# Performance work log

Measured on AMD Instinct MI355X. Metric: run time of the kernel, lower is better.

Reference implementation:

```python
import jax, jax.numpy as jnp
import numpy as np

FEATS = 1024
HEAD = 16
MLP_HIDDEN = 4096
HEAD_DIM = FEATS // HEAD
SQRT_D = float(FEATS) ** 0.5  # module scales by sqrt(feats), not sqrt(head_dim)
LN_EPS = 1e-5


def layer_norm(x, g, b):
    mu = jnp.mean(x, axis=-1, keepdims=True)
    var = jnp.mean(jnp.square(x - mu), axis=-1, keepdims=True)
    return (x - mu) * jax.lax.rsqrt(var + LN_EPS) * g + b


def setup_inputs() -> dict:
    key = jax.random.key(0)
    ks = jax.random.split(key, 12)
    s = 1.0 / np.sqrt(FEATS)
    s2 = 1.0 / np.sqrt(MLP_HIDDEN)
    return {
        "x": jax.random.normal(ks[0], (2, 2048, FEATS), dtype=jnp.float32),
        "ln1_g": jnp.ones((FEATS,), jnp.float32),
        "ln1_b": jnp.zeros((FEATS,), jnp.float32),
        "wq": jax.random.normal(ks[1], (FEATS, FEATS), jnp.float32) * s,
        "bq": jnp.zeros((FEATS,), jnp.float32),
        "wk": jax.random.normal(ks[2], (FEATS, FEATS), jnp.float32) * s,
        "bk": jnp.zeros((FEATS,), jnp.float32),
        "wv": jax.random.normal(ks[3], (FEATS, FEATS), jnp.float32) * s,
        "bv": jnp.zeros((FEATS,), jnp.float32),
        "wo": jax.random.normal(ks[4], (FEATS, FEATS), jnp.float32) * s,
        "bo": jnp.zeros((FEATS,), jnp.float32),
        "ln2_g": jnp.ones((FEATS,), jnp.float32),
        "ln2_b": jnp.zeros((FEATS,), jnp.float32),
        "w1": jax.random.normal(ks[5], (MLP_HIDDEN, FEATS), jnp.float32) * s,
        "b1": jnp.zeros((MLP_HIDDEN,), jnp.float32),
        "w2": jax.random.normal(ks[6], (FEATS, MLP_HIDDEN), jnp.float32) * s2,
        "b2": jnp.zeros((FEATS,), jnp.float32),
    }


def reference(x, ln1_g, ln1_b, wq, bq, wk, bk, wv, bv, wo, bo,
              ln2_g, ln2_b, w1, b1, w2, b2):
    b, n, f = x.shape
    h = layer_norm(x, ln1_g, ln1_b)
    # qkv projections (torch Linear: y = x @ W.T + b)
    q = (h @ wq.T + bq).reshape(b, n, HEAD, HEAD_DIM).transpose(0, 2, 1, 3)
    k = (h @ wk.T + bk).reshape(b, n, HEAD, HEAD_DIM).transpose(0, 2, 1, 3)
    v = (h @ wv.T + bv).reshape(b, n, HEAD, HEAD_DIM).transpose(0, 2, 1, 3)
    score = jax.nn.softmax(jnp.einsum('bhif,bhjf->bhij', q, k) / SQRT_D, axis=-1)
    attn = jnp.einsum('bhij,bhjf->bihf', score, v).reshape(b, n, f)
    o = attn @ wo.T + bo
    out1 = o + x
    h2 = layer_norm(out1, ln2_g, ln2_b)
    mlp = jax.nn.relu(jax.nn.relu(h2 @ w1.T + b1) @ w2.T + b2)
    return mlp + out1
```

## Files before the change

### kernel.cpp

```cpp
#include <hip/hip_runtime.h>
#include <hip/hip_bf16.h>

#define FEATS 1024
#define NH 16
#define HD 64
#define SEQ 2048
#define BATCH 2
#define MTOT (BATCH*SEQ)
#define MLPH 4096
#define QSCALE 0.04508422277369218f

typedef __attribute__((ext_vector_type(8))) short bf16x8;
typedef __attribute__((ext_vector_type(4))) short bf16x4;
typedef __attribute__((ext_vector_type(4))) float f32x4;

static_assert(sizeof(bf16x8) == 16, "bf16x8 must be 16B");

__device__ __forceinline__ unsigned short f2bf(float f) {
    unsigned int u = __float_as_uint(f);
    unsigned int lsb = (u >> 16) & 1u;
    u += 0x7fffu + lsb;
    return (unsigned short)(u >> 16);
}

#define ASYNC16(GP, LP) __builtin_amdgcn_global_load_lds( \
    (const __attribute__((address_space(1))) void*)(GP),  \
    (__attribute__((address_space(3))) void*)(LP), 16, 0, 0)

__global__ __launch_bounds__(256) void cvt_kernel(const float* __restrict__ src,
                                                  unsigned short* __restrict__ dst,
                                                  int n, float scale) {
    int i = (blockIdx.x * 256 + threadIdx.x) * 4;
    if (i + 3 < n) {
        float4 v = *(const float4*)(src + i);
        ushort4 o;
        o.x = f2bf(v.x * scale); o.y = f2bf(v.y * scale);
        o.z = f2bf(v.z * scale); o.w = f2bf(v.w * scale);
        *(ushort4*)(dst + i) = o;
    }
}

__global__ __launch_bounds__(256) void concat3_kernel(const float* __restrict__ a,
                                                      const float* __restrict__ b,
                                                      const float* __restrict__ c,
                                                      float* __restrict__ o) {
    int i = blockIdx.x * 256 + threadIdx.x;
    float v = (i < 1024) ? a[i] * QSCALE : ((i < 2048) ? b[i - 1024] : c[i - 2048]);
    o[i] = v;
}

__global__ __launch_bounds__(256) void ln_kernel(const float* __restrict__ x,
                                                 const float* __restrict__ g,
                                                 const float* __restrict__ bta,
                                                 unsigned short* __restrict__ h) {
    __shared__ float red[8];
    const int row = blockIdx.x;
    const int t = threadIdx.x;
    const float* xr = x + (size_t)row * FEATS;
    float4 v = ((const float4*)xr)[t];
    float s  = v.x + v.y + v.z + v.w;
    float ss = v.x * v.x + v.y * v.y + v.z * v.z + v.w * v.w;
#pragma unroll
    for (int off = 1; off < 64; off <<= 1) {
        s  += __shfl_xor(s, off);
        ss += __shfl_xor(ss, off);
    }
    const int w = t >> 6;
    if ((t & 63) == 0) { red[w] = s; red[4 + w] = ss; }
    __syncthreads();
    s  = red[0] + red[1] + red[2] + red[3];
    ss = red[4] + red[5] + red[6] + red[7];
    const float mu  = s * (1.f / FEATS);
    const float var = ss * (1.f / FEATS) - mu * mu;
    const float rs  = rsqrtf(var + 1e-5f);
    float4 gv = ((const float4*)g)[t];
    float4 bv = ((const float4*)bta)[t];
    ushort4 ov;
    ov.x = f2bf((v.x - mu) * rs * gv.x + bv.x);
    ov.y = f2bf((v.y - mu) * rs * gv.y + bv.y);
    ov.z = f2bf((v.z - mu) * rs * gv.z + bv.z);
    ov.w = f2bf((v.w - mu) * rs * gv.w + bv.w);
    ((ushort4*)h)[(size_t)row * (FEATS / 4) + t] = ov;
}

template <bool RELU, bool ADD, bool OUTBF16>
__global__ __launch_bounds__(256, 3)
void gemm_kernel(const unsigned short* __restrict__ A,
                 const unsigned short* __restrict__ W,
                 const float* __restrict__ bias,
                 const float* __restrict__ addend,
                 void* __restrict__ outp,
                 int M, int N, int K, int gx) {
    __shared__ unsigned short lds[3][2][128 * 32];

    const int t = threadIdx.x;
    const int w = t >> 6, lane = t & 63;
    const int wr = w >> 1, wc = w & 1;
    const int li = lane & 15, lj = lane >> 4;

    const int nwg = gridDim.x;
    const int cpx = nwg >> 3;
    const int wg = blockIdx.x;
    const int swz = (wg & 7) * cpx + (wg >> 3);
    const int mb = (swz / gx) * 128, nb = (swz % gx) * 128;

    const int srow = lane >> 2, sc = (lane & 3) * 8;
    const unsigned short* gA = A + (size_t)(mb + w * 16 + srow) * K + sc;
    const unsigned short* gB = W + (size_t)(nb + w * 16 + srow) * K + sc;
    const size_t half = (size_t)64 * K;
    const int lbase = w * 512 + lane * 8;

    const int nt = K >> 5;

#define STAGE(BUF, K0)                                             \
    do {                                                           \
        unsigned short* la_ = &lds[BUF][0][lbase];                 \
        unsigned short* lb_ = &lds[BUF][1][lbase];                 \
        ASYNC16(gA + (K0), la_);                                   \
        ASYNC16(gA + half + (K0), la_ + 2048);                     \
        ASYNC16(gB + (K0), lb_);                                   \
        ASYNC16(gB + half + (K0), lb_ + 2048);                     \
    } while (0)

    STAGE(0, 0);
    STAGE(1, 32);
    asm volatile("s_waitcnt vmcnt(4)" ::: "memory");
    __builtin_amdgcn_s_barrier();

    f32x4 acc[4][4] = {};

    for (int i = 0; i < nt; ++i) {
        const int cur = i % 3;
        const unsigned short* Al = &lds[cur][0][0];
        const unsigned short* Bl = &lds[cur][1][0];

        bf16x8 af[4], bfr[4];
#pragma unroll
        for (int m = 0; m < 4; m++)
            af[m] = *(const bf16x8*)(Al + (wr * 64 + m * 16 + li) * 32 + lj * 8);
#pragma unroll
        for (int n = 0; n < 4; n++)
            bfr[n] = *(const bf16x8*)(Bl + (wc * 64 + n * 16 + li) * 32 + lj * 8);

        const int pf = i + 2 < nt;
        if (pf) STAGE((i + 2) % 3, (i + 2) * 32);

#pragma unroll
        for (int m = 0; m < 4; m++)
#pragma unroll
            for (int n = 0; n < 4; n++)
                acc[m][n] = __builtin_amdgcn_mfma_f32_16x16x32_bf16(af[m], bfr[n], acc[m][n], 0, 0, 0);

        if (i + 1 < nt) {
            if (pf) asm volatile("s_waitcnt vmcnt(4)" ::: "memory");
            else    asm volatile("s_waitcnt vmcnt(0)" ::: "memory");
            __builtin_amdgcn_s_barrier();
        }
    }
#undef STAGE

#pragma unroll
    for (int m = 0; m < 4; m++) {
#pragma unroll
        for (int n = 0; n < 4; n++) {
            const int col = nb + wc * 64 + n * 16 + li;
            const float bv = bias[col];
#pragma unroll
            for (int r = 0; r < 4; r++) {
                const int row = mb + wr * 64 + m * 16 + lj * 4 + r;
                float v = acc[m][n][r] + bv;
                if (RELU) v = fmaxf(v, 0.f);
                if (ADD)  v += addend[(size_t)row * N + col];
                if (OUTBF16)
                    ((unsigned short*)outp)[(size_t)row * N + col] = f2bf(v);
                else
                    ((float*)outp)[(size_t)row * N + col] = v;
            }
        }
    }
}

__global__ __launch_bounds__(256) void vtrans_kernel(const unsigned short* __restrict__ qkv,
                                                     unsigned short* __restrict__ vt) {
    constexpr int LDV = 68;
    __shared__ unsigned short Vl[64 * LDV];
    const int bh = blockIdx.x, st = blockIdx.y;
    const int b = bh >> 4, h = bh & 15;
    const int t = threadIdx.x;
    const unsigned short* src = qkv + (size_t)(b * SEQ + st * 64) * (3 * FEATS) + 2 * FEATS + h * HD;
#pragma unroll
    for (int i = 0; i < 2; i++) {
        int idx = t + i * 256;
        int r = idx >> 3, c = (idx & 7) * 8;
        *(bf16x8*)(Vl + r * LDV + c) = *(const bf16x8*)(src + (size_t)r * (3 * FEATS) + c);
    }
    __syncthreads();
    unsigned short* dst = vt + (size_t)bh * HD * SEQ + st * 64;
#pragma unroll
    for (int i = 0; i < 2; i++) {
        int idx = t + i * 256;
        int d = idx >> 3, s8 = (idx & 7) * 8;
        bf16x8 v;
#pragma unroll
        for (int j = 0; j < 8; j++) v[j] = Vl[(s8 + j) * LDV + d];
        *(bf16x8*)(dst + (size_t)d * SEQ + s8) = v;
    }
}

__global__ __launch_bounds__(512, 4)
void attn_kernel(const unsigned short* __restrict__ qkv,
                 const unsigned short* __restrict__ vt,
                 unsigned short* __restrict__ out) {
    constexpr int LK = 72;
    constexpr int LV = 136;
    __shared__ unsigned short Kl[2][128 * LK];
    __shared__ unsigned short Vtl[2][64 * LV];

    const int bh = blockIdx.y;
    const int b = bh >> 4, h = bh & 15;
    const int q0 = blockIdx.x * 128;
    const int t = threadIdx.x, w = t >> 6, lane = t & 63;
    const int li = lane & 15, lj = lane >> 4;

    const size_t rstr = 3 * FEATS;
    const unsigned short* qkvb = qkv + (size_t)(b * SEQ) * rstr;
    const unsigned short* ksrc = qkvb + FEATS + h * HD;
    const unsigned short* vsrc = vt + (size_t)bh * HD * SEQ;

    bf16x8 aq[2];
#pragma unroll
    for (int kk = 0; kk < 2; kk++)
        aq[kk] = *(const bf16x8*)(qkvb + (size_t)(q0 + w * 16 + li) * rstr + h * HD + kk * 32 + lj * 8);

    f32x4 o[4] = {};
    float lsum = 0.f;

    const int skey = t >> 2, sc = (t & 3) * 16;
    const unsigned short* kg = ksrc + (size_t)skey * rstr + sc;
    const int ldoK = skey * LK + sc;
    const int sd = t >> 3, c0 = (t & 7) * 16;
    const unsigned short* vg = vsrc + (size_t)sd * SEQ + c0;
    const int posA = (c0 & 96) | (((c0 >> 2) & 3) << 3) | (((c0 >> 4) & 1) << 2);
    const int ldoV = sd * LV + posA;

    const int nt = SEQ / 128;

#define VSPLIT(VR0, VR1, BUF)                                            \
    do {                                                                 \
        *(bf16x4*)(&Vtl[BUF][ldoV])      = __builtin_shufflevector(VR0, VR0, 0, 1, 2, 3); \
        *(bf16x4*)(&Vtl[BUF][ldoV + 8])  = __builtin_shufflevector(VR0, VR0, 4, 5, 6, 7); \
        *(bf16x4*)(&Vtl[BUF][ldoV + 16]) = __builtin_shufflevector(VR1, VR1, 0, 1, 2, 3); \
        *(bf16x4*)(&Vtl[BUF][ldoV + 24]) = __builtin_shufflevector(VR1, VR1, 4, 5, 6, 7); \
    } while (0)

    {
        bf16x8 k0 = *(const bf16x8*)kg;
        bf16x8 k1 = *(const bf16x8*)(kg + 8);
        bf16x8 v0 = *(const bf16x8*)vg;
        bf16x8 v1 = *(const bf16x8*)(vg + 8);
        *(bf16x8*)(&Kl[0][ldoK])     = k0;
        *(bf16x8*)(&Kl[0][ldoK + 8]) = k1;
        VSPLIT(v0, v1, 0);
    }

    int cur = 0;
    for (int i = 0; i < nt; ++i) {
        bf16x8 kr0, kr1, vr0, vr1;
        if (i + 1 < nt) {
            const unsigned short* kn = kg + (size_t)(i + 1) * 128 * rstr;
            const unsigned short* vn = vg + (i + 1) * 128;
            kr0 = *(const bf16x8*)kn;
            kr1 = *(const bf16x8*)(kn + 8);
            vr0 = *(const bf16x8*)vn;
            vr1 = *(const bf16x8*)(vn + 8);
        }

        asm volatile("s_waitcnt lgkmcnt(0)" ::: "memory");
        __builtin_amdgcn_s_barrier();

        const unsigned short* Kc = Kl[cur];
        const unsigned short* Vc = Vtl[cur];

        f32x4 s[8];
        __builtin_amdgcn_s_setprio(1);
#pragma unroll
        for (int n = 0; n < 8; n++) {
            bf16x8 k0 = *(const bf16x8*)(Kc + (n * 16 + li) * LK + lj * 8);
            bf16x8 k1 = *(const bf16x8*)(Kc + (n * 16 + li) * LK + 32 + lj * 8);
            f32x4 acc = {};
            acc = __builtin_amdgcn_mfma_f32_16x16x32_bf16(k0, aq[0], acc, 0, 0, 0);
            acc = __builtin_amdgcn_mfma_f32_16x16x32_bf16(k1, aq[1], acc, 0, 0, 0);
            s[n] = acc;
        }
        __builtin_amdgcn_s_setprio(0);

        bf16x8 A[4];
#pragma unroll
        for (int kk = 0; kk < 4; kk++) {
            float p[8];
#pragma unroll
            for (int r = 0; r < 4; r++) {
                p[r]     = exp2f(s[2 * kk][r]);
                p[4 + r] = exp2f(s[2 * kk + 1][r]);
                lsum += p[r] + p[4 + r];
            }
            union { unsigned u[4]; bf16x8 v; } Au;
            asm("v_cvt_pk_bf16_f32 %0, %1, %2" : "=v"(Au.u[0]) : "v"(p[0]), "v"(p[1]));
            asm("v_cvt_pk_bf16_f32 %0, %1, %2" : "=v"(Au.u[1]) : "v"(p[2]), "v"(p[3]));
            asm("v_cvt_pk_bf16_f32 %0, %1, %2" : "=v"(Au.u[2]) : "v"(p[4]), "v"(p[5]));
            asm("v_cvt_pk_bf16_f32 %0, %1, %2" : "=v"(Au.u[3]) : "v"(p[6]), "v"(p[7]));
            A[kk] = Au.v;
        }

        __builtin_amdgcn_s_setprio(1);
#pragma unroll
        for (int n = 0; n < 4; n++) {
#pragma unroll
            for (int kk = 0; kk < 4; kk++) {
                bf16x8 bv = *(const bf16x8*)(Vc + (n * 16 + li) * LV + kk * 32 + lj * 8);
                o[n] = __builtin_amdgcn_mfma_f32_16x16x32_bf16(A[kk], bv, o[n], 0, 0, 0);
            }
        }
        __builtin_amdgcn_s_setprio(0);

        if (i + 1 < nt) {
            *(bf16x8*)(&Kl[cur ^ 1][ldoK])     = kr0;
            *(bf16x8*)(&Kl[cur ^ 1][ldoK + 8]) = kr1;
            VSPLIT(vr0, vr1, cur ^ 1);
        }
        cur ^= 1;
    }
#undef VSPLIT

    lsum += __shfl_xor(lsum, 16);
    lsum += __shfl_xor(lsum, 32);
    const float dinv = 1.f / lsum;
    float inv[4];
#pragma unroll
    for (int r = 0; r < 4; r++)
        inv[r] = __shfl(dinv, lj * 4 + r);

    unsigned short* ob = out + (size_t)(b * SEQ + q0 + w * 16) * FEATS + h * HD;
#pragma unroll
    for (int n = 0; n < 4; n++)
#pragma unroll
        for (int r = 0; r < 4; r++)
            ob[(size_t)(lj * 4 + r) * FEATS + n * 16 + li] = f2bf(o[n][r] * inv[r]);
}

extern "C" void kernel_launch(void* const* d_in, const int* in_sizes, int n_in,
                              void* d_out, int out_size, void* d_ws, size_t ws_size,
                              hipStream_t stream) {
    const float* x     = (const float*)d_in[0];
    const float* ln1_g = (const float*)d_in[1];
    const float* ln1_b = (const float*)d_in[2];
    const float* wq    = (const float*)d_in[3];
    const float* bq    = (const float*)d_in[4];
    const float* wk    = (const float*)d_in[5];
    const float* bk    = (const float*)d_in[6];
    const float* wv    = (const float*)d_in[7];
    const float* bvv   = (const float*)d_in[8];
    const float* wo    = (const float*)d_in[9];
    const float* bo    = (const float*)d_in[10];
    const float* ln2_g = (const float*)d_in[11];
    const float* ln2_b = (const float*)d_in[12];
    const float* w1    = (const float*)d_in[13];
    const float* b1    = (const float*)d_in[14];
    const float* w2    = (const float*)d_in[15];
    const float* b2    = (const float*)d_in[16];

    unsigned short* wqkv_b = (unsigned short*)d_ws;
    unsigned short* wo_b   = wqkv_b + 3072 * 1024;
    unsigned short* w1_b   = wo_b + 1024 * 1024;
    unsigned short* w2_b   = w1_b + 4096 * 1024;
    float*          bqkv   = (float*)(w2_b + 1024 * 4096);
    unsigned short* region = (unsigned short*)(bqkv + 3072);
    unsigned short* qkvb   = region;
    unsigned short* hb     = region + (size_t)4096 * 3072;
    unsigned short* vtb    = hb;
    unsigned short* a1     = region;
    unsigned short* attn_o = region + (size_t)4096 * 4096;
    unsigned short* h2     = attn_o;
    float*          out1   = (float*)(attn_o + (size_t)4096 * 1024);
    float*          outf   = (float*)d_out;

    dim3 blk(256);

    cvt_kernel<<<1024, blk, 0, stream>>>(wq, wqkv_b, 1024 * 1024, QSCALE);
    cvt_kernel<<<1024, blk, 0, stream>>>(wk, wqkv_b + 1024 * 1024, 1024 * 1024, 1.0f);
    cvt_kernel<<<1024, blk, 0, stream>>>(wv, wqkv_b + 2 * 1024 * 1024, 1024 * 1024, 1.0f);
    cvt_kernel<<<1024, blk, 0, stream>>>(wo, wo_b, 1024 * 1024, 1.0f);
    cvt_kernel<<<4096, blk, 0, stream>>>(w1, w1_b, 4096 * 1024, 1.0f);
    cvt_kernel<<<4096, blk, 0, stream>>>(w2, w2_b, 4096 * 1024, 1.0f);
    concat3_kernel<<<12, blk, 0, stream>>>(bq, bk, bvv, bqkv);

    ln_kernel<<<MTOT, blk, 0, stream>>>(x, ln1_g, ln1_b, hb);

    gemm_kernel<false, false, true><<<768, blk, 0, stream>>>(
        hb, wqkv_b, bqkv, nullptr, qkvb, MTOT, 3072, FEATS, 24);

    vtrans_kernel<<<dim3(BATCH * NH, SEQ / 64), blk, 0, stream>>>(qkvb, vtb);

    attn_kernel<<<dim3(SEQ / 128, BATCH * NH), dim3(512), 0, stream>>>(qkvb, vtb, attn_o);

    gemm_kernel<false, true, false><<<256, blk, 0, stream>>>(
        attn_o, wo_b, bo, x, out1, MTOT, FEATS, FEATS, 8);

    ln_kernel<<<MTOT, blk, 0, stream>>>(out1, ln2_g, ln2_b, h2);

    gemm_kernel<true, false, true><<<1024, blk, 0, stream>>>(
        h2, w1_b, b1, nullptr, a1, MTOT, MLPH, FEATS, 32);

    gemm_kernel<true, true, false><<<256, blk, 0, stream>>>(
        a1, w2_b, b2, out1, outf, MTOT, FEATS, MLPH, 8);
}
```

Baseline: 247.6 us.

## Fuse weight conversions, XOR-swizzle GEMM LDS tiles, reorder attention grid

Replaces the six per-weight fp32-to-bf16 conversion launches with one kernel that picks the source by flat index and writes into the contiguous bf16 weight workspace. The GEMM's async global-to-LDS loads and fragment reads use an XOR swizzle on the 8-element column chunk, which is meant to cut LDS bank conflicts. The attention grid is transposed so consecutive workgroups cover different heads rather than different query tiles of the same head, which changes cache locality and scheduling order. Each change is small, but the three are unrelated.

```diff
diff --git a/kernel.cpp b/kernel.cpp
--- a/kernel.cpp
+++ b/kernel.cpp
@@ -27,17 +27,27 @@
     (const __attribute__((address_space(1))) void*)(GP),  \
     (__attribute__((address_space(3))) void*)(LP), 16, 0, 0)
 
-__global__ __launch_bounds__(256) void cvt_kernel(const float* __restrict__ src,
-                                                  unsigned short* __restrict__ dst,
-                                                  int n, float scale) {
-    int i = (blockIdx.x * 256 + threadIdx.x) * 4;
-    if (i + 3 < n) {
-        float4 v = *(const float4*)(src + i);
-        ushort4 o;
-        o.x = f2bf(v.x * scale); o.y = f2bf(v.y * scale);
-        o.z = f2bf(v.z * scale); o.w = f2bf(v.w * scale);
-        *(ushort4*)(dst + i) = o;
-    }
+__global__ __launch_bounds__(256) void cvt_all_kernel(
+    const float* __restrict__ wq, const float* __restrict__ wk,
+    const float* __restrict__ wv, const float* __restrict__ wo,
+    const float* __restrict__ w1, const float* __restrict__ w2,
+    unsigned short* __restrict__ dst) {
+    const size_t i = ((size_t)blockIdx.x * 256 + threadIdx.x) * 4;
+    const size_t MB = (size_t)1024 * 1024;
+    const float* s;
+    size_t off;
+    float sc = 1.0f;
+    if (i < MB)            { s = wq; off = i;          sc = QSCALE; }
+    else if (i < 2 * MB)   { s = wk; off = i - MB; }
+    else if (i < 3 * MB)   { s = wv; off = i - 2 * MB; }
+    else if (i < 4 * MB)   { s = wo; off = i - 3 * MB; }
+    else if (i < 8 * MB)   { s = w1; off = i - 4 * MB; }
+    else                   { s = w2; off = i - 8 * MB; }
+    float4 v = *(const float4*)(s + off);
+    ushort4 o;
+    o.x = f2bf(v.x * sc); o.y = f2bf(v.y * sc);
+    o.z = f2bf(v.z * sc); o.w = f2bf(v.w * sc);
+    *(ushort4*)(dst + i) = o;
 }
 
 __global__ __launch_bounds__(256) void concat3_kernel(const float* __restrict__ a,
@@ -104,11 +114,14 @@
     const int swz = (wg & 7) * cpx + (wg >> 3);
     const int mb = (swz / gx) * 128, nb = (swz % gx) * 128;
 
-    const int srow = lane >> 2, sc = (lane & 3) * 8;
-    const unsigned short* gA = A + (size_t)(mb + w * 16 + srow) * K + sc;
-    const unsigned short* gB = W + (size_t)(nb + w * 16 + srow) * K + sc;
+    const int srow = lane >> 2;
+    const int scg = ((lane & 3) ^ (srow & 3)) * 8;
+    const unsigned short* gA = A + (size_t)(mb + w * 16 + srow) * K + scg;
+    const unsigned short* gB = W + (size_t)(nb + w * 16 + srow) * K + scg;
     const size_t half = (size_t)64 * K;
     const int lbase = w * 512 + lane * 8;
+
+    const int rsw = (lj ^ (li & 3)) * 8;
 
     const int nt = K >> 5;
 
@@ -137,10 +150,10 @@
         bf16x8 af[4], bfr[4];
 #pragma unroll
         for (int m = 0; m < 4; m++)
-            af[m] = *(const bf16x8*)(Al + (wr * 64 + m * 16 + li) * 32 + lj * 8);
+            af[m] = *(const bf16x8*)(Al + (wr * 64 + m * 16 + li) * 32 + rsw);
 #pragma unroll
         for (int n = 0; n < 4; n++)
-            bfr[n] = *(const bf16x8*)(Bl + (wc * 64 + n * 16 + li) * 32 + lj * 8);
+            bfr[n] = *(const bf16x8*)(Bl + (wc * 64 + n * 16 + li) * 32 + rsw);
 
         const int pf = i + 2 < nt;
         if (pf) STAGE((i + 2) % 3, (i + 2) * 32);
@@ -216,9 +229,9 @@
     __shared__ unsigned short Kl[2][128 * LK];
     __shared__ unsigned short Vtl[2][64 * LV];
 
-    const int bh = blockIdx.y;
+    const int bh = blockIdx.x;
     const int b = bh >> 4, h = bh & 15;
-    const int q0 = blockIdx.x * 128;
+    const int q0 = blockIdx.y * 128;
     const int t = threadIdx.x, w = t >> 6, lane = t & 63;
     const int li = lane & 15, lj = lane >> 4;
 
@@ -386,12 +399,7 @@
 
     dim3 blk(256);
 
-    cvt_kernel<<<1024, blk, 0, stream>>>(wq, wqkv_b, 1024 * 1024, QSCALE);
-    cvt_kernel<<<1024, blk, 0, stream>>>(wk, wqkv_b + 1024 * 1024, 1024 * 1024, 1.0f);
-    cvt_kernel<<<1024, blk, 0, stream>>>(wv, wqkv_b + 2 * 1024 * 1024, 1024 * 1024, 1.0f);
-    cvt_kernel<<<1024, blk, 0, stream>>>(wo, wo_b, 1024 * 1024, 1.0f);
-    cvt_kernel<<<4096, blk, 0, stream>>>(w1, w1_b, 4096 * 1024, 1.0f);
-    cvt_kernel<<<4096, blk, 0, stream>>>(w2, w2_b, 4096 * 1024, 1.0f);
+    cvt_all_kernel<<<12288, blk, 0, stream>>>(wq, wk, wv, wo, w1, w2, wqkv_b);
     concat3_kernel<<<12, blk, 0, stream>>>(bq, bk, bvv, bqkv);
 
     ln_kernel<<<MTOT, blk, 0, stream>>>(x, ln1_g, ln1_b, hb);
@@ -401,7 +409,7 @@
 
     vtrans_kernel<<<dim3(BATCH * NH, SEQ / 64), blk, 0, stream>>>(qkvb, vtb);
 
-    attn_kernel<<<dim3(SEQ / 128, BATCH * NH), dim3(512), 0, stream>>>(qkvb, vtb, attn_o);
+    attn_kernel<<<dim3(BATCH * NH, SEQ / 128), dim3(512), 0, stream>>>(qkvb, vtb, attn_o);
 
     gemm_kernel<false, true, false><<<256, blk, 0, stream>>>(
         attn_o, wo_b, bo, x, out1, MTOT, FEATS, FEATS, 8);
```

Result: faster. 236.0 us (-4.7%).
